# Optimization experiments

Measured on AMD Instinct MI355X. Metric: run time of the kernel, lower is better.

## Reference

```python
import jax, jax.numpy as jnp
import numpy as np

N = 2048
DIM_A = 256   # appearance feature dim (hardcoded 256 in WK/WQ/WV)
DIM_K = 64    # key_feature_dim
DIM_G = 64    # geo_feature_dim


def setup_inputs() -> dict:
    key = jax.random.key(0)
    ks = jax.random.split(key, 12)
    s = 0.05
    return {
        "f_a": jax.random.normal(ks[0], (N, DIM_A), dtype=jnp.float32),
        "position_embedding": jax.random.normal(ks[1], (N, N, DIM_G), dtype=jnp.float32),
        # torch nn.Linear weights are [out_features, in_features]
        "WG_w": jax.random.normal(ks[2], (1, DIM_G), dtype=jnp.float32) * s,
        "WG_b": jax.random.normal(ks[3], (1,), dtype=jnp.float32) * s,
        "WK_w": jax.random.normal(ks[4], (DIM_K, DIM_A), dtype=jnp.float32) * s,
        "WK_b": jax.random.normal(ks[5], (DIM_K,), dtype=jnp.float32) * s,
        "WQ_w": jax.random.normal(ks[6], (DIM_K, DIM_A), dtype=jnp.float32) * s,
        "WQ_b": jax.random.normal(ks[7], (DIM_K,), dtype=jnp.float32) * s,
        "WV_w": jax.random.normal(ks[8], (DIM_K, DIM_A), dtype=jnp.float32) * s,
        "WV_b": jax.random.normal(ks[9], (DIM_K,), dtype=jnp.float32) * s,
    }


def reference(f_a, position_embedding, WG_w, WG_b, WK_w, WK_b, WQ_w, WQ_b, WV_w, WV_b):
    n = f_a.shape[0]
    dim_k = WK_w.shape[0]
    dim_g = WG_w.shape[1]
    # geometric bias: relu(WG(g)), then log-clamp -> [N, N]
    w_g = jax.nn.relu(position_embedding.reshape(-1, dim_g) @ WG_w.T + WG_b).reshape(n, n)
    # projections of appearance features
    w_k = f_a @ WK_w.T + WK_b   # [N, dim_k]  (key index m)
    w_q = f_a @ WQ_w.T + WQ_b   # [N, dim_k]  (query index n)
    w_v = f_a @ WV_w.T + WV_b   # [N, dim_k]
    # scaled dot product: scores[m, n] = k_m . q_n / sqrt(dim_k)
    scaled_dot = (w_k @ w_q.T) / jnp.sqrt(jnp.asarray(dim_k, dtype=f_a.dtype))
    w_mn = jnp.log(jnp.clip(w_g, 1e-6)) + scaled_dot
    w_mn = jax.nn.softmax(w_mn, axis=1)        # softmax over dim=1 as in source
    # weighted sum of values along the softmax axis -> [N, dim_k]
    output = w_mn @ w_v
    return output
```

## Files before the change

kernel.cpp:

```cpp
#include <hip/hip_runtime.h>
#include <hip/hip_bf16.h>
#include <math.h>

#define NN 2048
#define DA 256
#define DK 64
#define DG 64
#define MROWS 4

typedef float f32x4 __attribute__((ext_vector_type(4)));

__device__ __forceinline__ float wave_reduce_max(float v) {
  #pragma unroll
  for (int o = 32; o >= 1; o >>= 1) v = fmaxf(v, __shfl_xor(v, o, 64));
  return v;
}
__device__ __forceinline__ float wave_reduce_sum(float v) {
  #pragma unroll
  for (int o = 32; o >= 1; o >>= 1) v += __shfl_xor(v, o, 64);
  return v;
}

__device__ __forceinline__ float dpp_reduce16(float x) {
  int t;
  t = __builtin_amdgcn_update_dpp(0, __float_as_int(x), 0xB1, 0xF, 0xF, true);
  x += __int_as_float(t);
  t = __builtin_amdgcn_update_dpp(0, __float_as_int(x), 0x4E, 0xF, 0xF, true);
  x += __int_as_float(t);
  t = __builtin_amdgcn_update_dpp(0, __float_as_int(x), 0x124, 0xF, 0xF, true);
  x += __int_as_float(t);
  t = __builtin_amdgcn_update_dpp(0, __float_as_int(x), 0x128, 0xF, 0xF, true);
  x += __int_as_float(t);
  return x;
}

__device__ __forceinline__ float dot4(const f32x4 a, const f32x4 b) {
  float d = a.x * b.x;
  d = fmaf(a.y, b.y, d);
  d = fmaf(a.z, b.z, d);
  d = fmaf(a.w, b.w, d);
  return d;
}

__global__ __launch_bounds__(256) void proj_kernel(
    const float* __restrict__ fa,
    const float* __restrict__ WKw, const float* __restrict__ WKb,
    const float* __restrict__ WQw, const float* __restrict__ WQb,
    const float* __restrict__ WVw, const float* __restrict__ WVb,
    float* __restrict__ wk, float* __restrict__ wq, float* __restrict__ wv)
{
  __shared__ float s_fa[DA];
  const int m = blockIdx.x, tid = threadIdx.x;
  s_fa[tid] = fa[(size_t)m * DA + tid];
  __syncthreads();
  if (tid < 192) {
    const int o = tid >> 6, k = tid & 63;
    const float* W = (o == 0 ? WKw : (o == 1 ? WQw : WVw)) + (size_t)k * DA;
    const float* B = (o == 0 ? WKb : (o == 1 ? WQb : WVb));
    float acc = B[k];
    const float4* W4 = (const float4*)W;
    const float4* F4 = (const float4*)s_fa;
    #pragma unroll 8
    for (int c = 0; c < DA / 4; ++c) {
      float4 w4 = W4[c], f4 = F4[c];
      acc = fmaf(w4.x, f4.x, acc); acc = fmaf(w4.y, f4.y, acc);
      acc = fmaf(w4.z, f4.z, acc); acc = fmaf(w4.w, f4.w, acc);
    }
    float* dst = (o == 0 ? wk : (o == 1 ? wq : wv));
    dst[(size_t)m * DK + k] = acc;
  }
}

__global__ __launch_bounds__(256) void fused_kernel(
    const float* __restrict__ pe,
    const float* __restrict__ wgw, const float* __restrict__ wgb,
    const float* __restrict__ wk, const float* __restrict__ wq,
    const float* __restrict__ wv,
    float* __restrict__ out)
{
  __shared__ float s_sc[MROWS][NN];
  __shared__ float s_pacc[4][MROWS][DK];
  __shared__ float s_rsum[MROWS];

  const int m0 = blockIdx.x * MROWS;
  const int tid = threadIdx.x;
  const int wave = tid >> 6, lane = tid & 63;
  const int sub = lane >> 4;
  const int c4  = lane & 15;

  {
    float acc[8][MROWS];
    #pragma unroll
    for (int j = 0; j < 8; ++j)
      #pragma unroll
      for (int i = 0; i < MROWS; ++i) acc[j][i] = 0.f;
    #pragma unroll 4
    for (int c = 0; c < DK / 4; ++c) {
      f32x4 wkc[MROWS];
      #pragma unroll
      for (int i = 0; i < MROWS; ++i)
        wkc[i] = ((const f32x4*)(wk + (size_t)(m0 + i) * DK))[c];
      #pragma unroll
      for (int j = 0; j < 8; ++j) {
        const int n = j * 256 + tid;
        const f32x4 q = ((const f32x4*)(wq + (size_t)n * DK))[c];
        #pragma unroll
        for (int i = 0; i < MROWS; ++i) {
          acc[j][i] = fmaf(q.x, wkc[i].x, acc[j][i]);
          acc[j][i] = fmaf(q.y, wkc[i].y, acc[j][i]);
          acc[j][i] = fmaf(q.z, wkc[i].z, acc[j][i]);
          acc[j][i] = fmaf(q.w, wkc[i].w, acc[j][i]);
        }
      }
    }
    #pragma unroll
    for (int j = 0; j < 8; ++j) {
      const int n = j * 256 + tid;
      #pragma unroll
      for (int i = 0; i < MROWS; ++i)
        s_sc[i][n] = acc[j][i] * 0.125f;
    }
  }
  __syncthreads();

  const f32x4 wg4 = ((const f32x4*)wgw)[c4];
  const float gb = wgb[0];
  const int n0w = wave * (NN / 4);
  #pragma unroll 2
  for (int it = 0; it < (NN / 4) / 4; ++it) {
    const int nb = n0w + it * 4;
    f32x4 p[MROWS];
    #pragma unroll
    for (int i = 0; i < MROWS; ++i)
      p[i] = __builtin_nontemporal_load(
          (const f32x4*)(pe + ((size_t)(m0 + i) * NN + nb) * DG) + lane);
    #pragma unroll
    for (int i = 0; i < MROWS; ++i) {
      float dg = dot4(p[i], wg4);
      dg = dpp_reduce16(dg);
      if (c4 == 0) {
        s_sc[i][nb + sub] += __logf(fmaxf(dg + gb, 1e-6f));
      }
    }
  }
  __syncthreads();

  {
    float mx = -INFINITY;
    #pragma unroll
    for (int j = 0; j < NN / 64; ++j)
      mx = fmaxf(mx, s_sc[wave][j * 64 + lane]);
    mx = wave_reduce_max(mx);
    float sm = 0.f;
    #pragma unroll
    for (int j = 0; j < NN / 64; ++j) {
      const float pr = __expf(s_sc[wave][j * 64 + lane] - mx);
      s_sc[wave][j * 64 + lane] = pr;
      sm += pr;
    }
    sm = wave_reduce_sum(sm);
    if (lane == 0) s_rsum[wave] = sm;
  }
  __syncthreads();

  f32x4 vacc[MROWS];
  #pragma unroll
  for (int i = 0; i < MROWS; ++i) vacc[i] = (f32x4){0.f, 0.f, 0.f, 0.f};
  #pragma unroll 4
  for (int it = 0; it < (NN / 4) / 4; ++it) {
    const int n = n0w + it * 4 + sub;
    const f32x4 v = ((const f32x4*)(wv + (size_t)n * DK))[c4];
    #pragma unroll
    for (int i = 0; i < MROWS; ++i) {
      const float pr = s_sc[i][n];
      vacc[i].x = fmaf(pr, v.x, vacc[i].x);
      vacc[i].y = fmaf(pr, v.y, vacc[i].y);
      vacc[i].z = fmaf(pr, v.z, vacc[i].z);
      vacc[i].w = fmaf(pr, v.w, vacc[i].w);
    }
  }
  #pragma unroll
  for (int i = 0; i < MROWS; ++i) {
    vacc[i].x += __shfl_xor(vacc[i].x, 16, 64); vacc[i].x += __shfl_xor(vacc[i].x, 32, 64);
    vacc[i].y += __shfl_xor(vacc[i].y, 16, 64); vacc[i].y += __shfl_xor(vacc[i].y, 32, 64);
    vacc[i].z += __shfl_xor(vacc[i].z, 16, 64); vacc[i].z += __shfl_xor(vacc[i].z, 32, 64);
    vacc[i].w += __shfl_xor(vacc[i].w, 16, 64); vacc[i].w += __shfl_xor(vacc[i].w, 32, 64);
  }
  if (lane < 16) {
    #pragma unroll
    for (int i = 0; i < MROWS; ++i)
      ((f32x4*)s_pacc[wave][i])[c4] = vacc[i];
  }
  __syncthreads();
  {
    const int i = tid >> 6, k = tid & 63;
    const float r = s_pacc[0][i][k] + s_pacc[1][i][k] +
                    s_pacc[2][i][k] + s_pacc[3][i][k];
    out[(size_t)(m0 + i) * DK + k] = r / s_rsum[i];
  }
}

extern "C" void kernel_launch(void* const* d_in, const int* in_sizes, int n_in,
                              void* d_out, int out_size, void* d_ws, size_t ws_size,
                              hipStream_t stream) {
  const float* fa  = (const float*)d_in[0];
  const float* pe  = (const float*)d_in[1];
  const float* wgw = (const float*)d_in[2];
  const float* wgb = (const float*)d_in[3];
  const float* wkw = (const float*)d_in[4];
  const float* wkb = (const float*)d_in[5];
  const float* wqw = (const float*)d_in[6];
  const float* wqb = (const float*)d_in[7];
  const float* wvw = (const float*)d_in[8];
  const float* wvb = (const float*)d_in[9];
  float* out = (float*)d_out;

  float* wk = (float*)d_ws;
  float* wq = wk + (size_t)NN * DK;
  float* wv = wq + (size_t)NN * DK;

  proj_kernel<<<NN, 256, 0, stream>>>(fa, wkw, wkb, wqw, wqb, wvw, wvb, wk, wq, wv);
  fused_kernel<<<NN / MROWS, 256, 0, stream>>>(pe, wgw, wgb, wk, wq, wv, out);
}
```

Before: 280.9 us.

## Process eight rows per 512-thread block and stream position embeddings contiguously

Each block now handles 8 query rows with 512 threads (8 waves) instead of 4 rows with 256 threads. This halves the number of times the wq and wv tables are re-read across the grid. The position-embedding pass becomes one flat loop over contiguous 1KB chunks interleaved across waves, so each wave issues a single sequential stream. The cost is 64KB of shared memory per block, more accumulator registers, and fewer blocks, which can lower occupancy for what is mainly a bandwidth-bound stream over position_embedding.

```diff
diff --git a/kernel.cpp b/kernel.cpp
--- a/kernel.cpp
+++ b/kernel.cpp
@@ -6,7 +6,8 @@
 #define DA 256
 #define DK 64
 #define DG 64
-#define MROWS 4
+#define MR 8
+#define TPB 512
 
 typedef float f32x4 __attribute__((ext_vector_type(4)));
 
@@ -71,41 +72,41 @@
   }
 }
 
-__global__ __launch_bounds__(256) void fused_kernel(
+__global__ __launch_bounds__(512) void fused_kernel(
     const float* __restrict__ pe,
     const float* __restrict__ wgw, const float* __restrict__ wgb,
     const float* __restrict__ wk, const float* __restrict__ wq,
     const float* __restrict__ wv,
     float* __restrict__ out)
 {
-  __shared__ float s_sc[MROWS][NN];
-  __shared__ float s_pacc[4][MROWS][DK];
-  __shared__ float s_rsum[MROWS];
-
-  const int m0 = blockIdx.x * MROWS;
+  __shared__ float s_sc[MR][NN];
+  __shared__ float s_pacc[8][MR][DK];
+  __shared__ float s_rsum[MR];
+
+  const int m0 = blockIdx.x * MR;
   const int tid = threadIdx.x;
   const int wave = tid >> 6, lane = tid & 63;
   const int sub = lane >> 4;
   const int c4  = lane & 15;
 
   {
-    float acc[8][MROWS];
-    #pragma unroll
-    for (int j = 0; j < 8; ++j)
-      #pragma unroll
-      for (int i = 0; i < MROWS; ++i) acc[j][i] = 0.f;
+    float acc[NN / TPB][MR];
+    #pragma unroll
+    for (int j = 0; j < NN / TPB; ++j)
+      #pragma unroll
+      for (int i = 0; i < MR; ++i) acc[j][i] = 0.f;
     #pragma unroll 4
     for (int c = 0; c < DK / 4; ++c) {
-      f32x4 wkc[MROWS];
-      #pragma unroll
-      for (int i = 0; i < MROWS; ++i)
+      f32x4 wkc[MR];
+      #pragma unroll
+      for (int i = 0; i < MR; ++i)
         wkc[i] = ((const f32x4*)(wk + (size_t)(m0 + i) * DK))[c];
       #pragma unroll
-      for (int j = 0; j < 8; ++j) {
-        const int n = j * 256 + tid;
+      for (int j = 0; j < NN / TPB; ++j) {
+        const int n = j * TPB + tid;
         const f32x4 q = ((const f32x4*)(wq + (size_t)n * DK))[c];
         #pragma unroll
-        for (int i = 0; i < MROWS; ++i) {
+        for (int i = 0; i < MR; ++i) {
           acc[j][i] = fmaf(q.x, wkc[i].x, acc[j][i]);
           acc[j][i] = fmaf(q.y, wkc[i].y, acc[j][i]);
           acc[j][i] = fmaf(q.z, wkc[i].z, acc[j][i]);
@@ -114,10 +115,10 @@
       }
     }
     #pragma unroll
-    for (int j = 0; j < 8; ++j) {
-      const int n = j * 256 + tid;
-      #pragma unroll
-      for (int i = 0; i < MROWS; ++i)
+    for (int j = 0; j < NN / TPB; ++j) {
+      const int n = j * TPB + tid;
+      #pragma unroll
+      for (int i = 0; i < MR; ++i)
         s_sc[i][n] = acc[j][i] * 0.125f;
     }
   }
@@ -125,22 +126,17 @@
 
   const f32x4 wg4 = ((const f32x4*)wgw)[c4];
   const float gb = wgb[0];
-  const int n0w = wave * (NN / 4);
-  #pragma unroll 2
-  for (int it = 0; it < (NN / 4) / 4; ++it) {
-    const int nb = n0w + it * 4;
-    f32x4 p[MROWS];
-    #pragma unroll
-    for (int i = 0; i < MROWS; ++i)
-      p[i] = __builtin_nontemporal_load(
-          (const f32x4*)(pe + ((size_t)(m0 + i) * NN + nb) * DG) + lane);
-    #pragma unroll
-    for (int i = 0; i < MROWS; ++i) {
-      float dg = dot4(p[i], wg4);
-      dg = dpp_reduce16(dg);
-      if (c4 == 0) {
-        s_sc[i][nb + sub] += __logf(fmaxf(dg + gb, 1e-6f));
-      }
+  const f32x4* peb = (const f32x4*)(pe + (size_t)m0 * NN * DG);
+  #pragma unroll 4
+  for (int it = 0; it < (MR * NN / 4) / 8; ++it) {
+    const int ch = it * 8 + wave;
+    const f32x4 p = __builtin_nontemporal_load(peb + (size_t)ch * 64 + lane);
+    const int i  = ch >> 9;
+    const int nb = (ch & 511) * 4;
+    float dg = dot4(p, wg4);
+    dg = dpp_reduce16(dg);
+    if (c4 == 0) {
+      s_sc[i][nb + sub] += __logf(fmaxf(dg + gb, 1e-6f));
     }
   }
   __syncthreads();
@@ -163,15 +159,16 @@
   }
   __syncthreads();
 
-  f32x4 vacc[MROWS];
-  #pragma unroll
-  for (int i = 0; i < MROWS; ++i) vacc[i] = (f32x4){0.f, 0.f, 0.f, 0.f};
+  f32x4 vacc[MR];
+  #pragma unroll
+  for (int i = 0; i < MR; ++i) vacc[i] = (f32x4){0.f, 0.f, 0.f, 0.f};
+  const int nbase = wave * (NN / 8);
   #pragma unroll 4
-  for (int it = 0; it < (NN / 4) / 4; ++it) {
-    const int n = n0w + it * 4 + sub;
+  for (int it = 0; it < (NN / 8) / 4; ++it) {
+    const int n = nbase + it * 4 + sub;
     const f32x4 v = ((const f32x4*)(wv + (size_t)n * DK))[c4];
     #pragma unroll
-    for (int i = 0; i < MROWS; ++i) {
+    for (int i = 0; i < MR; ++i) {
       const float pr = s_sc[i][n];
       vacc[i].x = fmaf(pr, v.x, vacc[i].x);
       vacc[i].y = fmaf(pr, v.y, vacc[i].y);
@@ -180,7 +177,7 @@
     }
   }
   #pragma unroll
-  for (int i = 0; i < MROWS; ++i) {
+  for (int i = 0; i < MR; ++i) {
     vacc[i].x += __shfl_xor(vacc[i].x, 16, 64); vacc[i].x += __shfl_xor(vacc[i].x, 32, 64);
     vacc[i].y += __shfl_xor(vacc[i].y, 16, 64); vacc[i].y += __shfl_xor(vacc[i].y, 32, 64);
     vacc[i].z += __shfl_xor(vacc[i].z, 16, 64); vacc[i].z += __shfl_xor(vacc[i].z, 32, 64);
@@ -188,14 +185,15 @@
   }
   if (lane < 16) {
     #pragma unroll
-    for (int i = 0; i < MROWS; ++i)
+    for (int i = 0; i < MR; ++i)
       ((f32x4*)s_pacc[wave][i])[c4] = vacc[i];
   }
   __syncthreads();
   {
     const int i = tid >> 6, k = tid & 63;
-    const float r = s_pacc[0][i][k] + s_pacc[1][i][k] +
-                    s_pacc[2][i][k] + s_pacc[3][i][k];
+    float r = 0.f;
+    #pragma unroll
+    for (int w = 0; w < 8; ++w) r += s_pacc[w][i][k];
     out[(size_t)(m0 + i) * DK + k] = r / s_rsum[i];
   }
 }
@@ -220,5 +218,5 @@
   float* wv = wq + (size_t)NN * DK;
 
   proj_kernel<<<NN, 256, 0, stream>>>(fa, wkw, wkb, wqw, wqb, wvw, wvb, wk, wq, wv);
-  fused_kernel<<<NN / MROWS, 256, 0, stream>>>(pe, wgw, wgb, wk, wq, wv, out);
-}
+  fused_kernel<<<NN / MR, TPB, 0, stream>>>(pe, wgw, wgb, wk, wq, wv, out);
+}
```

New measurement: 405.7 us. +44.4%, slower.
